# Optimization experiments

Measured on AMD Instinct MI355X. Metric: run time of the kernel, lower is better.

## Reference

```python
import jax, jax.numpy as jnp
import numpy as np

N_NODES = 100000
N_EDGES = 3200000
EMB = 128
HID = 128
N_CLASS = 10
N_SHAPE = 16
N_COLOR = 16
MAX_POS = 150000
N_GRAPH = 1024


def setup_inputs() -> dict:
    key = jax.random.key(0)
    ks = jax.random.split(key, 12)
    node_feats = jax.random.randint(ks[0], (N_NODES, 3), 0, N_SHAPE, dtype=jnp.int64 if jax.config.jax_enable_x64 else jnp.int32)
    edge_index = jax.random.randint(ks[1], (2, N_EDGES), 0, N_NODES)
    batch = jnp.sort(jax.random.randint(ks[2], (N_NODES,), 0, N_GRAPH))
    s = 0.02
    shape_emb = jax.random.normal(ks[3], (N_SHAPE, EMB), jnp.float32) * s
    color_emb = jax.random.normal(ks[4], (N_COLOR, EMB), jnp.float32) * s
    pos_emb = jax.random.normal(ks[5], (MAX_POS, EMB), jnp.float32) * s
    w1_l = jax.random.normal(ks[6], (HID, EMB), jnp.float32) / np.sqrt(EMB)
    b1_l = jnp.zeros((HID,), jnp.float32)
    w1_r = jax.random.normal(ks[7], (HID, EMB), jnp.float32) / np.sqrt(EMB)
    w2_l = jax.random.normal(ks[8], (HID, HID), jnp.float32) / np.sqrt(HID)
    b2_l = jnp.zeros((HID,), jnp.float32)
    w2_r = jax.random.normal(ks[9], (HID, HID), jnp.float32) / np.sqrt(HID)
    lin_w = jax.random.normal(ks[10], (N_CLASS, HID), jnp.float32) / np.sqrt(HID)
    lin_b = jnp.zeros((N_CLASS,), jnp.float32)
    return {"node_feats": node_feats, "edge_index": edge_index, "batch": batch,
            "shape_emb": shape_emb, "color_emb": color_emb, "pos_emb": pos_emb,
            "w1_l": w1_l, "b1_l": b1_l, "w1_r": w1_r,
            "w2_l": w2_l, "b2_l": b2_l, "w2_r": w2_r,
            "lin_w": lin_w, "lin_b": lin_b}


def _sage_conv(x, src, dst, deg_inv, w_l, b_l, w_r):
    # mean-aggregate neighbor features: gather x[src], scatter-add at dst, divide by degree
    msg_sum = jax.ops.segment_sum(x[src], dst, num_segments=N_NODES)  # [N, D]
    agg = msg_sum * deg_inv[:, None]
    # PyG SAGEConv: lin_l(aggr) + lin_r(x); bias lives in lin_l
    return agg @ w_l.T + b_l + x @ w_r.T


def reference(node_feats, edge_index, batch, shape_emb, color_emb, pos_emb,
              w1_l, b1_l, w1_r, w2_l, b2_l, w2_r, lin_w, lin_b):
    s, c, p = node_feats[:, 0], node_feats[:, 1], node_feats[:, 2]
    x = shape_emb[s] + color_emb[c] + pos_emb[p]            # [N, EMB]
    src, dst = edge_index[0], edge_index[1]
    deg = jax.ops.segment_sum(jnp.ones((N_EDGES,), x.dtype), dst, num_segments=N_NODES)
    deg_inv = jnp.where(deg > 0, 1.0 / jnp.maximum(deg, 1.0), 0.0)
    x = jax.nn.relu(_sage_conv(x, src, dst, deg_inv, w1_l, b1_l, w1_r))
    x = jax.nn.relu(_sage_conv(x, src, dst, deg_inv, w2_l, b2_l, w2_r))
    # global mean pool over graphs
    pooled_sum = jax.ops.segment_sum(x, batch, num_segments=N_GRAPH)  # [G, HID]
    counts = jax.ops.segment_sum(jnp.ones((N_NODES,), x.dtype), batch, num_segments=N_GRAPH)
    pooled = pooled_sum / jnp.maximum(counts, 1.0)[:, None]
    return pooled @ lin_w.T + lin_b                          # [G, N_CLASS]
```

## Files before the change

### kernel.cpp

```cpp
#include <hip/hip_runtime.h>

#define N_NODES 100000
#define N_EDGES 3200000
#define EMB 128
#define N_GRAPH 1024
#define N_CLASS 10
#define CAP 96

#define EPB 5120
#define NBLK_E (N_EDGES / EPB)
#define NBK 391
#define NTOT (NBK * NBLK_E)
#define SCAN_B 1024
#define NB_SCAN ((NTOT + SCAN_B - 1) / SCAN_B)

#define EMBED_BLKS (N_NODES * 16 / 256)
#define WCAT_BLKS 256

typedef unsigned int uint32;
typedef __attribute__((ext_vector_type(8))) short bf16x8;
typedef __attribute__((ext_vector_type(4))) float f32x4;
typedef __attribute__((ext_vector_type(2))) float f32x2;

__device__ inline unsigned short f2bf(float f) {
  unsigned u = __float_as_uint(f);
  u += 0x7fffu + ((u >> 16) & 1u);
  return (unsigned short)(u >> 16);
}
__device__ inline float bf2f(unsigned short s) {
  return __uint_as_float(((unsigned)s) << 16);
}
__device__ inline unsigned char f2fp8(float v) {
  return (unsigned char)(__builtin_amdgcn_cvt_pk_fp8_f32(v, v, 0, false) & 0xff);
}

__global__ __launch_bounds__(256) void k_hist(
    const int* __restrict__ dst, int* __restrict__ counts,
    const int* __restrict__ nf, const float* __restrict__ se,
    const float* __restrict__ ce, const float* __restrict__ pe,
    unsigned short* __restrict__ X, unsigned char* __restrict__ X8,
    const float* __restrict__ w1l, const float* __restrict__ w1r,
    const float* __restrict__ w2l, const float* __restrict__ w2r,
    unsigned short* __restrict__ wc1, unsigned short* __restrict__ wc2) {
  int b = blockIdx.x;
  int tid = threadIdx.x;
  if (b < NBLK_E) {
    __shared__ int h[NBK];
    for (int i = tid; i < NBK; i += 256) h[i] = 0;
    __syncthreads();
    int base = b * EPB;
#pragma unroll
    for (int it = 0; it < 20; ++it) {
      int d = dst[base + it * 256 + tid];
      atomicAdd(&h[d >> 8], 1);
    }
    __syncthreads();
    for (int i = tid; i < NBK; i += 256) counts[i * NBLK_E + b] = h[i];
  } else if (b < NBLK_E + EMBED_BLKS) {
    int gid = (b - NBLK_E) * 256 + tid;
    int node = gid >> 4;
    int q = (gid & 15) * 8;
    int s = nf[node * 3 + 0];
    int c = nf[node * 3 + 1];
    int p = nf[node * 3 + 2];
    const float* ps = se + s * EMB + q;
    const float* pc = ce + c * EMB + q;
    const float* pp = pe + p * EMB + q;
    float4 a0 = *(const float4*)ps, a1 = *(const float4*)(ps + 4);
    float4 b0 = *(const float4*)pc, b1 = *(const float4*)(pc + 4);
    float4 d0 = *(const float4*)pp, d1 = *(const float4*)(pp + 4);
    float r0 = a0.x + b0.x + d0.x, r1 = a0.y + b0.y + d0.y;
    float r2 = a0.z + b0.z + d0.z, r3 = a0.w + b0.w + d0.w;
    float r4 = a1.x + b1.x + d1.x, r5 = a1.y + b1.y + d1.y;
    float r6 = a1.z + b1.z + d1.z, r7 = a1.w + b1.w + d1.w;
    uint4 o;
    o.x = (uint32)f2bf(r0) | ((uint32)f2bf(r1) << 16);
    o.y = (uint32)f2bf(r2) | ((uint32)f2bf(r3) << 16);
    o.z = (uint32)f2bf(r4) | ((uint32)f2bf(r5) << 16);
    o.w = (uint32)f2bf(r6) | ((uint32)f2bf(r7) << 16);
    *(uint4*)(X + (size_t)node * EMB + q) = o;
    int w0 = __builtin_amdgcn_cvt_pk_fp8_f32(r0, r1, 0, false);
    w0 = __builtin_amdgcn_cvt_pk_fp8_f32(r2, r3, w0, true);
    int w1 = __builtin_amdgcn_cvt_pk_fp8_f32(r4, r5, 0, false);
    w1 = __builtin_amdgcn_cvt_pk_fp8_f32(r6, r7, w1, true);
    uint2 o8;
    o8.x = (uint32)w0;
    o8.y = (uint32)w1;
    *(uint2*)(X8 + (size_t)node * EMB + q) = o8;
  } else {
    int wb = b - (NBLK_E + EMBED_BLKS);
    const float* wl = (wb < 128) ? w1l : w2l;
    const float* wr = (wb < 128) ? w1r : w2r;
    unsigned short* wcat = (wb < 128) ? wc1 : wc2;
    int gid = (wb & 127) * 256 + tid;
    int j = gid >> 8;
    int k = gid & 255;
    float v = (k < EMB) ? wl[j * EMB + k] : wr[j * EMB + (k - EMB)];
    wcat[gid] = f2bf(v);
  }
}

__global__ void k_scan1(int* __restrict__ data, int* __restrict__ part) {
  __shared__ int t[SCAN_B];
  int tid = threadIdx.x;
  int gid = blockIdx.x * SCAN_B + tid;
  int v = (gid < NTOT) ? data[gid] : 0;
  t[tid] = v;
  __syncthreads();
  for (int s = 1; s < SCAN_B; s <<= 1) {
    int u = (tid >= s) ? t[tid - s] : 0;
    __syncthreads();
    t[tid] += u;
    __syncthreads();
  }
  if (gid < NTOT) data[gid] = t[tid] - v;
  if (tid == SCAN_B - 1) part[blockIdx.x] = t[tid];
}

__global__ void k_scan2(int* __restrict__ part) {
  __shared__ int t[512];
  int tid = threadIdx.x;
  int v = (tid < NB_SCAN) ? part[tid] : 0;
  t[tid] = v;
  __syncthreads();
  for (int s = 1; s < 512; s <<= 1) {
    int u = (tid >= s) ? t[tid - s] : 0;
    __syncthreads();
    t[tid] += u;
    __syncthreads();
  }
  if (tid < NB_SCAN) part[tid] = t[tid] - v;
}

__global__ void k_scanf(int* __restrict__ data, const int* __restrict__ part) {
  int gid = blockIdx.x * SCAN_B + threadIdx.x;
  if (gid < NTOT) data[gid] += part[gid >> 10];
}

__global__ __launch_bounds__(256) void k_part(const int* __restrict__ src,
                                              const int* __restrict__ dst,
                                              const int* __restrict__ scanned,
                                              uint32* __restrict__ psort) {
  __shared__ int h[NBK];
  int b = blockIdx.x;
  int tid = threadIdx.x;
  for (int i = tid; i < NBK; i += 256) h[i] = 0;
  __syncthreads();
  int base = b * EPB;
#pragma unroll
  for (int it = 0; it < 20; ++it) {
    int e = base + it * 256 + tid;
    int d = dst[e];
    int s = src[e];
    int r = atomicAdd(&h[d >> 8], 1);
    int pos = scanned[(d >> 8) * NBLK_E + b] + r;
    psort[pos] = ((uint32)(d & 255) << 24) | (uint32)s;
  }
}

__global__ __launch_bounds__(256) void k_csr(const uint32* __restrict__ psort,
                                             const int* __restrict__ scanned,
                                             int* __restrict__ csrp,
                                             int* __restrict__ degi) {
  __shared__ int h[256];
  int b = blockIdx.x;
  int tid = threadIdx.x;
  h[tid] = 0;
  __syncthreads();
  int start = scanned[b * NBLK_E];
  int end = (b == NBK - 1) ? N_EDGES : scanned[(b + 1) * NBLK_E];
  for (int e = start + tid; e < end; e += 256) {
    uint32 p = psort[e];
    int dl = (int)(p >> 24);
    int s = (int)(p & 0xFFFFFFu);
    int r = atomicAdd(&h[dl], 1);
    csrp[(size_t)(b * 256 + dl) * CAP + r] = s;
  }
  __syncthreads();
  int node = b * 256 + tid;
  if (node < N_NODES) degi[node] = h[tid];
}

__global__ __launch_bounds__(256) void k_agg(const unsigned char* __restrict__ in8,
                                             unsigned short* __restrict__ out,
                                             const int* __restrict__ degi,
                                             const int* __restrict__ csrp) {
  int grp = threadIdx.x >> 4;
  int l16 = threadIdx.x & 15;
  int node = blockIdx.x * 16 + grp;
  size_t start = (size_t)node * CAP;
  int cnt = degi[node];
  const unsigned char* base = in8 + l16 * 8;
  f32x2 a0 = {0.f, 0.f}, a1 = {0.f, 0.f}, a2 = {0.f, 0.f}, a3 = {0.f, 0.f};
  int i = 0;
  for (; i + 8 <= cnt; i += 8) {
    int s0 = csrp[start + i + 0];
    int s1 = csrp[start + i + 1];
    int s2 = csrp[start + i + 2];
    int s3 = csrp[start + i + 3];
    int s4 = csrp[start + i + 4];
    int s5 = csrp[start + i + 5];
    int s6 = csrp[start + i + 6];
    int s7 = csrp[start + i + 7];
    uint2 v0 = *(const uint2*)(base + (size_t)s0 * EMB);
    uint2 v1 = *(const uint2*)(base + (size_t)s1 * EMB);
    uint2 v2 = *(const uint2*)(base + (size_t)s2 * EMB);
    uint2 v3 = *(const uint2*)(base + (size_t)s3 * EMB);
    uint2 v4 = *(const uint2*)(base + (size_t)s4 * EMB);
    uint2 v5 = *(const uint2*)(base + (size_t)s5 * EMB);
    uint2 v6 = *(const uint2*)(base + (size_t)s6 * EMB);
    uint2 v7 = *(const uint2*)(base + (size_t)s7 * EMB);
#define ACC(v)                                                   \
    a0 += __builtin_amdgcn_cvt_pk_f32_fp8((int)v.x, false);      \
    a1 += __builtin_amdgcn_cvt_pk_f32_fp8((int)v.x, true);       \
    a2 += __builtin_amdgcn_cvt_pk_f32_fp8((int)v.y, false);      \
    a3 += __builtin_amdgcn_cvt_pk_f32_fp8((int)v.y, true);
    ACC(v0) ACC(v1) ACC(v2) ACC(v3) ACC(v4) ACC(v5) ACC(v6) ACC(v7)
  }
  for (; i < cnt; ++i) {
    int s = csrp[start + i];
    uint2 v = *(const uint2*)(base + (size_t)s * EMB);
    ACC(v)
  }
#undef ACC
  float di = cnt > 0 ? 1.0f / (float)cnt : 0.0f;
  uint4 o;
  o.x = (uint32)f2bf(a0.x * di) | ((uint32)f2bf(a0.y * di) << 16);
  o.y = (uint32)f2bf(a1.x * di) | ((uint32)f2bf(a1.y * di) << 16);
  o.z = (uint32)f2bf(a2.x * di) | ((uint32)f2bf(a2.y * di) << 16);
  o.w = (uint32)f2bf(a3.x * di) | ((uint32)f2bf(a3.y * di) << 16);
  *(uint4*)(out + (size_t)node * EMB + l16 * 8) = o;
}

__global__ __launch_bounds__(512) void k_gemm(const unsigned short* __restrict__ A,
                                              const unsigned short* __restrict__ S,
                                              const unsigned short* __restrict__ Wcat,
                                              const float* __restrict__ bias,
                                              unsigned short* __restrict__ out,
                                              unsigned char* __restrict__ out8) {
  __shared__ unsigned char ldsW[65536];
  int tid = threadIdx.x;
  {
    const uint4* w4 = (const uint4*)Wcat;
#pragma unroll
    for (int it = 0; it < 8; ++it) {
      int i = tid + it * 512;
      uint4 v = w4[i];
      unsigned a = (unsigned)i << 4;
      a ^= ((a >> 9) & 7u) << 4;
      *(uint4*)(ldsW + a) = v;
    }
  }
  __syncthreads();

  int wid = tid >> 6;
  int lane = tid & 63;
  int rows0 = blockIdx.x * 128 + wid * 16;
  int r = lane & 15;
  int khalf = lane >> 4;
  int arow = rows0 + r;
  if (arow > N_NODES - 1) arow = N_NODES - 1;
  const unsigned short* Abase = A + (size_t)arow * EMB + khalf * 8;
  const unsigned short* Sbase = S + (size_t)arow * EMB + khalf * 8;
  unsigned bswz = ((unsigned)(r & 7)) << 4;

  f32x4 acc[8] = {};
#pragma unroll
  for (int kc = 0; kc < 8; ++kc) {
    const unsigned short* p = (kc < 4) ? (Abase + kc * 32) : (Sbase + (kc - 4) * 32);
    bf16x8 a = *(const bf16x8*)p;
#pragma unroll
    for (int jc = 0; jc < 8; ++jc) {
      unsigned addr = (((unsigned)(jc * 16 + r)) << 9) + ((unsigned)kc << 6) +
                      ((unsigned)khalf << 4);
      bf16x8 b = *(const bf16x8*)(ldsW + (addr ^ bswz));
      acc[jc] = __builtin_amdgcn_mfma_f32_16x16x32_bf16(a, b, acc[jc], 0, 0, 0);
    }
  }

  int rbase = (lane >> 4) * 4;
#pragma unroll
  for (int jc = 0; jc < 8; ++jc) {
    int col = jc * 16 + r;
    float bv = bias[col];
#pragma unroll
    for (int q = 0; q < 4; ++q) {
      int row = rows0 + rbase + q;
      if (row < N_NODES) {
        float v = fmaxf(acc[jc][q] + bv, 0.f);
        out[(size_t)row * EMB + col] = f2bf(v);
        if (out8) out8[(size_t)row * EMB + col] = f2fp8(v);
      }
    }
  }
}

__global__ void k_pool(const unsigned short* __restrict__ h, const int* __restrict__ batch,
                       const float* __restrict__ lw, const float* __restrict__ lb,
                       float* __restrict__ out) {
  int g = blockIdx.x;
  int tid = threadIdx.x;
  int lo = 0, hi = N_NODES;
  while (lo < hi) {
    int mid = (lo + hi) >> 1;
    if (batch[mid] < g) lo = mid + 1; else hi = mid;
  }
  int lo2 = lo, hi2 = N_NODES;
  while (lo2 < hi2) {
    int mid = (lo2 + hi2) >> 1;
    if (batch[mid] < g + 1) lo2 = mid + 1; else hi2 = mid;
  }
  float sum = 0.f;
  for (int n = lo; n < lo2; ++n) sum += bf2f(h[(size_t)n * EMB + tid]);
  int cnt = lo2 - lo;
  float pooled = sum / fmaxf((float)cnt, 1.0f);
  __shared__ float pl[EMB];
  pl[tid] = pooled;
  __syncthreads();
  if (tid < N_CLASS) {
    float o = lb[tid];
    for (int d = 0; d < EMB; ++d) o += pl[d] * lw[tid * EMB + d];
    out[g * N_CLASS + tid] = o;
  }
}

extern "C" void kernel_launch(void* const* d_in, const int* in_sizes, int n_in,
                              void* d_out, int out_size, void* d_ws, size_t ws_size,
                              hipStream_t stream) {
  const int* nf = (const int*)d_in[0];
  const int* ei = (const int*)d_in[1];
  const int* batch = (const int*)d_in[2];
  const float* se = (const float*)d_in[3];
  const float* ce = (const float*)d_in[4];
  const float* pe = (const float*)d_in[5];
  const float* w1l = (const float*)d_in[6];
  const float* b1l = (const float*)d_in[7];
  const float* w1r = (const float*)d_in[8];
  const float* w2l = (const float*)d_in[9];
  const float* b2l = (const float*)d_in[10];
  const float* w2r = (const float*)d_in[11];
  const float* linw = (const float*)d_in[12];
  const float* linb = (const float*)d_in[13];
  float* out = (float*)d_out;

  char* ws = (char*)d_ws;
  size_t off = 0;
  auto alloc = [&](size_t bytes) {
    void* p = ws + off;
    off = (off + bytes + 255) & ~(size_t)255;
    return p;
  };
  unsigned short* X = (unsigned short*)alloc((size_t)N_NODES * EMB * 2);
  unsigned short* H = (unsigned short*)alloc((size_t)N_NODES * EMB * 2);
  unsigned short* X2 = (unsigned short*)alloc((size_t)N_NODES * EMB * 2);
  unsigned short* AGG = (unsigned short*)alloc((size_t)N_NODES * EMB * 2);
  unsigned char* X8 = (unsigned char*)alloc((size_t)N_NODES * EMB);
  unsigned char* H8 = (unsigned char*)alloc((size_t)N_NODES * EMB);
  unsigned short* WC1 = (unsigned short*)alloc((size_t)256 * EMB * 2);
  unsigned short* WC2 = (unsigned short*)alloc((size_t)256 * EMB * 2);
  int* degi = (int*)alloc((size_t)N_NODES * 4);
  int* counts = (int*)alloc((size_t)NTOT * 4);
  int* part = (int*)alloc((size_t)512 * 4);
  uint32* psort = (uint32*)alloc((size_t)N_EDGES * 4);
  int* csrp = (int*)alloc((size_t)N_NODES * CAP * 4);

  const int* srcv = ei;
  const int* dstv = ei + N_EDGES;

  k_hist<<<NBLK_E + EMBED_BLKS + WCAT_BLKS, 256, 0, stream>>>(
      dstv, counts, nf, se, ce, pe, X, X8, w1l, w1r, w2l, w2r, WC1, WC2);
  k_scan1<<<NB_SCAN, SCAN_B, 0, stream>>>(counts, part);
  k_scan2<<<1, 512, 0, stream>>>(part);
  k_scanf<<<NB_SCAN, SCAN_B, 0, stream>>>(counts, part);
  k_part<<<NBLK_E, 256, 0, stream>>>(srcv, dstv, counts, psort);
  k_csr<<<NBK, 256, 0, stream>>>(psort, counts, csrp, degi);

  k_agg<<<N_NODES / 16 + 1, 256, 0, stream>>>(X8, AGG, degi, csrp);
  k_gemm<<<(N_NODES + 127) / 128, 512, 0, stream>>>(AGG, X, WC1, b1l, H, H8);
  k_agg<<<N_NODES / 16 + 1, 256, 0, stream>>>(H8, AGG, degi, csrp);
  k_gemm<<<(N_NODES + 127) / 128, 512, 0, stream>>>(AGG, H, WC2, b2l, X2, nullptr);
  k_pool<<<N_GRAPH, EMB, 0, stream>>>(X2, batch, linw, linb, out);
}
```

Baseline: 288.1 us.

## Shrink edge partition blocks and fold scan fixup into partition kernels

Reduces edges per histogram/partition block from 5120 to 1280, so four times as many blocks run the histogram and scatter phases. The scan's final add kernel is removed: partition and CSR kernels add the block partial sums on the fly, with partition caching its scanned column in shared memory. The second-level scan grows to 1024 entries to cover the larger count array, which makes the counts array and scan work four times larger.

```diff
diff --git a/kernel.cpp b/kernel.cpp
--- a/kernel.cpp
+++ b/kernel.cpp
@@ -7,7 +7,7 @@
 #define N_CLASS 10
 #define CAP 96
 
-#define EPB 5120
+#define EPB 1280
 #define NBLK_E (N_EDGES / EPB)
 #define NBK 391
 #define NTOT (NBK * NBLK_E)
@@ -50,7 +50,7 @@
     __syncthreads();
     int base = b * EPB;
 #pragma unroll
-    for (int it = 0; it < 20; ++it) {
+    for (int it = 0; it < 5; ++it) {
       int d = dst[base + it * 256 + tid];
       atomicAdd(&h[d >> 8], 1);
     }
@@ -118,48 +118,49 @@
 }
 
 __global__ void k_scan2(int* __restrict__ part) {
-  __shared__ int t[512];
+  __shared__ int t[1024];
   int tid = threadIdx.x;
   int v = (tid < NB_SCAN) ? part[tid] : 0;
   t[tid] = v;
   __syncthreads();
-  for (int s = 1; s < 512; s <<= 1) {
+  for (int s = 1; s < 1024; s <<= 1) {
     int u = (tid >= s) ? t[tid - s] : 0;
     __syncthreads();
     t[tid] += u;
     __syncthreads();
   }
   if (tid < NB_SCAN) part[tid] = t[tid] - v;
-}
-
-__global__ void k_scanf(int* __restrict__ data, const int* __restrict__ part) {
-  int gid = blockIdx.x * SCAN_B + threadIdx.x;
-  if (gid < NTOT) data[gid] += part[gid >> 10];
 }
 
 __global__ __launch_bounds__(256) void k_part(const int* __restrict__ src,
                                               const int* __restrict__ dst,
-                                              const int* __restrict__ scanned,
+                                              const int* __restrict__ counts,
+                                              const int* __restrict__ part,
                                               uint32* __restrict__ psort) {
   __shared__ int h[NBK];
+  __shared__ int scol[NBK];
   int b = blockIdx.x;
   int tid = threadIdx.x;
-  for (int i = tid; i < NBK; i += 256) h[i] = 0;
+  for (int i = tid; i < NBK; i += 256) {
+    h[i] = 0;
+    int idx = i * NBLK_E + b;
+    scol[i] = counts[idx] + part[idx >> 10];
+  }
   __syncthreads();
   int base = b * EPB;
 #pragma unroll
-  for (int it = 0; it < 20; ++it) {
+  for (int it = 0; it < 5; ++it) {
     int e = base + it * 256 + tid;
     int d = dst[e];
     int s = src[e];
     int r = atomicAdd(&h[d >> 8], 1);
-    int pos = scanned[(d >> 8) * NBLK_E + b] + r;
-    psort[pos] = ((uint32)(d & 255) << 24) | (uint32)s;
+    psort[scol[d >> 8] + r] = ((uint32)(d & 255) << 24) | (uint32)s;
   }
 }
 
 __global__ __launch_bounds__(256) void k_csr(const uint32* __restrict__ psort,
-                                             const int* __restrict__ scanned,
+                                             const int* __restrict__ counts,
+                                             const int* __restrict__ part,
                                              int* __restrict__ csrp,
                                              int* __restrict__ degi) {
   __shared__ int h[256];
@@ -167,8 +168,13 @@
   int tid = threadIdx.x;
   h[tid] = 0;
   __syncthreads();
-  int start = scanned[b * NBLK_E];
-  int end = (b == NBK - 1) ? N_EDGES : scanned[(b + 1) * NBLK_E];
+  int i0 = b * NBLK_E;
+  int start = counts[i0] + part[i0 >> 10];
+  int end = N_EDGES;
+  if (b != NBK - 1) {
+    int i1 = (b + 1) * NBLK_E;
+    end = counts[i1] + part[i1 >> 10];
+  }
   for (int e = start + tid; e < end; e += 256) {
     uint32 p = psort[e];
     int dl = (int)(p >> 24);
@@ -360,7 +366,7 @@
   unsigned short* WC2 = (unsigned short*)alloc((size_t)256 * EMB * 2);
   int* degi = (int*)alloc((size_t)N_NODES * 4);
   int* counts = (int*)alloc((size_t)NTOT * 4);
-  int* part = (int*)alloc((size_t)512 * 4);
+  int* part = (int*)alloc((size_t)1024 * 4);
   uint32* psort = (uint32*)alloc((size_t)N_EDGES * 4);
   int* csrp = (int*)alloc((size_t)N_NODES * CAP * 4);
 
@@ -370,10 +376,9 @@
   k_hist<<<NBLK_E + EMBED_BLKS + WCAT_BLKS, 256, 0, stream>>>(
       dstv, counts, nf, se, ce, pe, X, X8, w1l, w1r, w2l, w2r, WC1, WC2);
   k_scan1<<<NB_SCAN, SCAN_B, 0, stream>>>(counts, part);
-  k_scan2<<<1, 512, 0, stream>>>(part);
-  k_scanf<<<NB_SCAN, SCAN_B, 0, stream>>>(counts, part);
-  k_part<<<NBLK_E, 256, 0, stream>>>(srcv, dstv, counts, psort);
-  k_csr<<<NBK, 256, 0, stream>>>(psort, counts, csrp, degi);
+  k_scan2<<<1, 1024, 0, stream>>>(part);
+  k_part<<<NBLK_E, 256, 0, stream>>>(srcv, dstv, counts, part, psort);
+  k_csr<<<NBK, 256, 0, stream>>>(psort, counts, part, csrp, degi);
 
   k_agg<<<N_NODES / 16 + 1, 256, 0, stream>>>(X8, AGG, degi, csrp);
   k_gemm<<<(N_NODES + 127) / 128, 512, 0, stream>>>(AGG, X, WC1, b1l, H, H8);
```

Result: slower. 295.5 us (+2.6%).
